# Optimization experiments

Hardware: AMD Instinct MI355X
Metric: run time of the kernel (lower is better)

The kernel has to match this reference:

```python
import jax, jax.numpy as jnp
import numpy as np

N_HEADS = 16
D_HEAD = 64
TAU = 30.0
NEG = -1e9


def setup_inputs() -> dict:
    key = jax.random.key(0)
    k1, k2, k3, k4 = jax.random.split(key, 4)
    B, L, D = 2, 2048, 1024
    scale = 1.0 / np.sqrt(D)
    return {
        "input": jax.random.normal(k1, (B, L, D), dtype=jnp.float32),
        "attention_mask": jnp.ones((B, L), dtype=jnp.int32),
        "W_Q": jax.random.normal(k2, (N_HEADS * D_HEAD, D), dtype=jnp.float32) * scale,
        "W_K": jax.random.normal(k3, (N_HEADS * D_HEAD, D), dtype=jnp.float32) * scale,
        "W_V": jax.random.normal(k4, (N_HEADS * D_HEAD, D), dtype=jnp.float32) * scale,
    }


def reference(input, attention_mask, W_Q, W_K, W_V):
    B, L, D = input.shape
    # fused QKV projection (F.linear: x @ W.T), split into heads: [B, H, L, Dh]
    def proj(W):
        return jnp.einsum('bld,ed->ble', input, W).reshape(B, L, N_HEADS, D_HEAD).transpose(0, 2, 1, 3)
    q, k, v = proj(W_Q), proj(W_K), proj(W_V)
    S = jnp.einsum('bhqd,bhkd->bhqk', q, k) / np.sqrt(D_HEAD)  # [B,H,L,L]
    S = TAU * jnp.tanh(S)
    causal = jnp.tril(jnp.ones((L, L), dtype=bool))            # True = keep
    keep = causal[None, None, :, :] & (attention_mask[:, None, None, :] != 0)
    S = jnp.where(keep, S, NEG)
    attn = jax.nn.softmax(S, axis=-1)
    out = jnp.einsum('bhqk,bhkd->bhqd', attn, v)
    return out.transpose(0, 2, 1, 3).reshape(B, L, N_HEADS * D_HEAD)
```

## Files before the change

kernel.cpp:

```cpp
#include <hip/hip_runtime.h>


typedef unsigned short u16;
typedef __bf16 bf16x8 __attribute__((ext_vector_type(8)));
typedef float f32x4 __attribute__((ext_vector_type(4)));

#define MFMA(a, b, c) __builtin_amdgcn_mfma_f32_16x16x32_bf16(a, b, c, 0, 0, 0)

__device__ __forceinline__ u16 bf16rne(float f) {
    unsigned int u = __float_as_uint(f);
    u += 0x7fffu + ((u >> 16) & 1u);
    return (u16)(u >> 16);
}
__device__ __forceinline__ float bf16f(u16 h) {
    return __uint_as_float(((unsigned int)h) << 16);
}
__device__ __forceinline__ void split1(float f, u16& hi, u16& lo) {
    hi = bf16rne(f);
    lo = bf16rne(f - bf16f(hi));
}

__device__ __forceinline__ void gl16(const u16* g, u16* l) {
    __builtin_amdgcn_global_load_lds(
        (const __attribute__((address_space(1))) unsigned int*)g,
        (__attribute__((address_space(3))) unsigned int*)l, 16, 0, 0);
}

__global__ __launch_bounds__(256) void presplit(
    const float* __restrict__ X, const float* __restrict__ Wq,
    const float* __restrict__ Wk, const float* __restrict__ Wv,
    u16* __restrict__ Xh, u16* __restrict__ Xl,
    u16* __restrict__ Wqh, u16* __restrict__ Wql,
    u16* __restrict__ Wkh, u16* __restrict__ Wkl,
    u16* __restrict__ Wvh)
{
    int i = blockIdx.x * 256 + threadIdx.x;
    const float* src; u16 *dh, *dl; int off;
    if (i < 1048576)      { src = X;  dh = Xh;  dl = Xl;      off = i; }
    else if (i < 1310720) { src = Wq; dh = Wqh; dl = Wql;     off = i - 1048576; }
    else if (i < 1572864) { src = Wk; dh = Wkh; dl = Wkl;     off = i - 1310720; }
    else                  { src = Wv; dh = Wvh; dl = nullptr; off = i - 1572864; }
    float4 v = ((const float4*)src)[off];
    ushort4 h, l;
    split1(v.x, h.x, l.x); split1(v.y, h.y, l.y);
    split1(v.z, h.z, l.z); split1(v.w, h.w, l.w);
    ((ushort4*)dh)[off] = h;
    if (dl) ((ushort4*)dl)[off] = l;
}

__global__ __launch_bounds__(256, 4) void qkv_gemm(
    const u16* __restrict__ Xh, const u16* __restrict__ Xl,
    const u16* __restrict__ Wqh, const u16* __restrict__ Wql,
    const u16* __restrict__ Wkh, const u16* __restrict__ Wkl,
    const u16* __restrict__ Wvh,
    u16* __restrict__ Qh, u16* __restrict__ Ql,
    u16* __restrict__ Kh, u16* __restrict__ Kl,
    u16* __restrict__ VT)
{
    __shared__ __align__(16) u16 Xhs[4096];
    __shared__ __align__(16) u16 Xls[4096];
    __shared__ __align__(16) u16 Whs[4096];
    __shared__ __align__(16) u16 Wls[4096];
    const int tid = threadIdx.x;
    const int wave = tid >> 6, lane = tid & 63, quad = lane >> 4, c16 = lane & 15;
    const int id = blockIdx.x;
    const int nb = (((id >> 3) % 3) << 3) | (id & 7);
    const int m0 = ((id >> 3) / 3) * 128;
    const int mat = nb >> 3;
    const int n0 = (nb & 7) * 128;
    const u16* Bh = (mat == 0) ? Wqh : ((mat == 1) ? Wkh : Wvh);
    const u16* Bl = (mat == 0) ? Wql : Wkl;
    const int nseg = (mat < 2) ? 3 : 1;
    const int wm = (wave >> 1) * 64, wn = (wave & 1) * 64;

    const int srow0 = wave * 32 + (lane >> 2), scol = (lane & 3) * 8;

    f32x4 acc[4][4];
#pragma unroll
    for (int i = 0; i < 4; i++)
#pragma unroll
        for (int j = 0; j < 4; j++) acc[i][j] = (f32x4){0.f, 0.f, 0.f, 0.f};

    for (int kt = 0; kt < 32; kt++) {
        const int kcol = kt * 32;
#pragma unroll
        for (int s = 0; s < 2; s++) {
            int row = srow0 + s * 16;
            size_t go = (size_t)row * 1024 + kcol + scol;
            int lo = row * 32 + scol;
            gl16(Xh + (size_t)m0 * 1024 + go, &Xhs[lo]);
            gl16(Bh + (size_t)n0 * 1024 + go, &Whs[lo]);
            if (nseg == 3) {
                gl16(Xl + (size_t)m0 * 1024 + go, &Xls[lo]);
                gl16(Bl + (size_t)n0 * 1024 + go, &Wls[lo]);
            }
        }
        __syncthreads();
        for (int seg = 0; seg < nseg; seg++) {
            const u16* ap = (seg < 2) ? Xhs : Xls;
            const u16* bp = (seg == 1) ? Wls : Whs;
            bf16x8 af[4], bfr[4];
#pragma unroll
            for (int mt = 0; mt < 4; mt++)
                af[mt] = *(const bf16x8*)&ap[(wm + mt * 16 + c16) * 32 + quad * 8];
#pragma unroll
            for (int nt = 0; nt < 4; nt++)
                bfr[nt] = *(const bf16x8*)&bp[(wn + nt * 16 + c16) * 32 + quad * 8];
#pragma unroll
            for (int mt = 0; mt < 4; mt++)
#pragma unroll
                for (int nt = 0; nt < 4; nt++)
                    acc[mt][nt] = MFMA(af[mt], bfr[nt], acc[mt][nt]);
        }
        __syncthreads();
    }

    const float scale = (mat == 0) ? 0.125f : 1.f;
#pragma unroll
    for (int mt = 0; mt < 4; mt++) {
#pragma unroll
        for (int nt = 0; nt < 4; nt++) {
#pragma unroll
            for (int reg = 0; reg < 4; reg++) {
                int mm = m0 + wm + mt * 16 + quad * 4 + reg;
                int n = n0 + wn + nt * 16 + c16;
                int b_ = mm >> 11, l = mm & 2047;
                int h = n >> 6, dh = n & 63;
                float v = acc[mt][nt][reg] * scale;
                if (mat == 2) {
                    VT[((b_ * 16 + h) * 64 + dh) * 2048 + l] = bf16rne(v);
                } else {
                    u16 hi, lo; split1(v, hi, lo);
                    int idx = ((b_ * 16 + h) * 2048 + l) * 64 + dh;
                    if (mat == 0) { Qh[idx] = hi; Ql[idx] = lo; }
                    else          { Kh[idx] = hi; Kl[idx] = lo; }
                }
            }
        }
    }
}

__global__ __launch_bounds__(256, 4) void attn(
    const u16* __restrict__ Qh, const u16* __restrict__ Ql,
    const u16* __restrict__ Kh, const u16* __restrict__ Kl,
    const u16* __restrict__ VT, const int* __restrict__ AM,
    u16* __restrict__ Op, float* __restrict__ Lp)
{
    __shared__ __align__(16) u16 Khs[2][4096];
    __shared__ __align__(16) u16 Kls[2][4096];
    __shared__ __align__(16) u16 Ps[4096];

    const int tid = threadIdx.x, wave = tid >> 6, lane = tid & 63;
    const int quad = lane >> 4, c16 = lane & 15;
    const int bh = blockIdx.x;
    const int pr = blockIdx.y;
    const int sp = blockIdx.z;
    const int b_ = bh >> 4;
    const size_t base = (size_t)bh * 2048 * 64;

    const int swsub[2] = { (wave * 2) >> 2, (wave * 2 + 1) >> 2 };
    const int swrow[2] = { ((wave * 2) & 3) * 16 + (lane >> 2), ((wave * 2 + 1) & 3) * 16 + (lane >> 2) };
    const int scol = (lane & 3) * 8;

    auto stageK = [&](int k0, int buf) {
        const u16* Kht = Kh + base + (size_t)k0 * 64;
        const u16* Klt = Kl + base + (size_t)k0 * 64;
#pragma unroll
        for (int s = 0; s < 2; s++) {
            int sub = swsub[s], row = swrow[s];
            int lo = sub * 2048 + row * 32 + scol;
            gl16(Kht + (size_t)row * 64 + sub * 32 + scol, &Khs[buf][lo]);
            gl16(Klt + (size_t)row * 64 + sub * 32 + scol, &Kls[buf][lo]);
        }
    };

    for (int tix = 0; tix < 2; ++tix) {
        const int qt = tix ? pr : 31 - pr;
        const int q0 = qt * 64;

        const size_t qrow = base + (size_t)(q0 + wave * 16 + c16) * 64 + quad * 8;
        bf16x8 qh0 = *(const bf16x8*)&Qh[qrow];
        bf16x8 qh1 = *(const bf16x8*)&Qh[qrow + 32];
        bf16x8 ql0 = *(const bf16x8*)&Ql[qrow];
        bf16x8 ql1 = *(const bf16x8*)&Ql[qrow + 32];

        float rsl[4] = {0.f, 0.f, 0.f, 0.f};
        f32x4 o[4];
#pragma unroll
        for (int r = 0; r < 4; r++) o[r] = (f32x4){0.f, 0.f, 0.f, 0.f};

        if (sp <= qt) {
            stageK(sp * 64, 0);
            int cur = 0;
            for (int kb = sp; kb <= qt; kb += 2) {
                const int k0 = kb * 64;
                __syncthreads();
                if (kb + 2 <= qt) stageK(k0 + 128, cur ^ 1);
                const int mkv = AM[b_ * 2048 + k0 + lane];
                const bool interior = (kb < qt);

                float p[4][4];
#pragma unroll
                for (int nt = 0; nt < 4; nt++) {
                    bf16x8 kh0 = *(const bf16x8*)&Khs[cur][(nt * 16 + c16) * 32 + quad * 8];
                    bf16x8 kh1 = *(const bf16x8*)&Khs[cur][2048 + (nt * 16 + c16) * 32 + quad * 8];
                    bf16x8 kl0 = *(const bf16x8*)&Kls[cur][(nt * 16 + c16) * 32 + quad * 8];
                    bf16x8 kl1 = *(const bf16x8*)&Kls[cur][2048 + (nt * 16 + c16) * 32 + quad * 8];
                    f32x4 sa = (f32x4){0.f, 0.f, 0.f, 0.f};
                    sa = MFMA(qh0, kh0, sa);
                    sa = MFMA(qh1, kh1, sa);
                    sa = MFMA(ql0, kh0, sa);
                    sa = MFMA(ql1, kh1, sa);
                    sa = MFMA(qh0, kl0, sa);
                    sa = MFMA(qh1, kl1, sa);
                    const int key = k0 + nt * 16 + c16;
                    const bool mok = (__shfl(mkv, nt * 16 + c16) != 0);
#pragma unroll
                    for (int reg = 0; reg < 4; reg++) {
                        int qg = q0 + wave * 16 + quad * 4 + reg;
                        float x = sa[reg];
                        float e1 = __expf(2.f * x);
                        float r  = __builtin_amdgcn_rcpf(e1 + 1.f);
                        float pv = __expf(-60.f * r);
                        bool keep = mok && (interior || key <= qg);
                        pv = keep ? pv : 0.f;
                        p[nt][reg] = pv;
                        rsl[reg] += pv;
                    }
                }

#pragma unroll
                for (int nt = 0; nt < 4; nt++) {
                    int kl_ = nt * 16 + c16, sub = kl_ >> 5, kc = kl_ & 31;
#pragma unroll
                    for (int reg = 0; reg < 4; reg++)
                        Ps[sub * 2048 + (wave * 16 + quad * 4 + reg) * 32 + kc] = bf16rne(p[nt][reg]);
                }
                bf16x8 p0 = *(const bf16x8*)&Ps[(wave * 16 + c16) * 32 + quad * 8];
                bf16x8 p1 = *(const bf16x8*)&Ps[2048 + (wave * 16 + c16) * 32 + quad * 8];

#pragma unroll
                for (int dt = 0; dt < 4; dt++) {
                    const size_t vrow = (size_t)(bh * 64 + dt * 16 + c16) * 2048 + k0 + quad * 8;
                    bf16x8 v0 = *(const bf16x8*)&VT[vrow];
                    bf16x8 v1 = *(const bf16x8*)&VT[vrow + 32];
                    o[dt] = MFMA(p0, v0, o[dt]);
                    o[dt] = MFMA(p1, v1, o[dt]);
                }
                cur ^= 1;
            }
        }
        __syncthreads();

        const size_t ob = ((size_t)(sp * 512 + bh * 16) + 0) * 0 +
                          ((size_t)((sp * 32 + 0) ) * 0);
        (void)ob;
        const size_t obase = (((size_t)sp * 1024 + (size_t)bh * 32 + qt) * 4096);
        const size_t lbase = (((size_t)sp * 1024 + (size_t)bh * 32 + qt) * 64);
        float lsum[4];
#pragma unroll
        for (int reg = 0; reg < 4; reg++) {
            float v = rsl[reg];
#pragma unroll
            for (int off = 1; off < 16; off <<= 1)
                v += __shfl_xor(v, off);
            lsum[reg] = v;
        }
        if (c16 == 0) {
#pragma unroll
            for (int reg = 0; reg < 4; reg++)
                Lp[lbase + wave * 16 + quad * 4 + reg] = lsum[reg];
        }
#pragma unroll
        for (int dt = 0; dt < 4; dt++)
#pragma unroll
            for (int reg = 0; reg < 4; reg++) {
                int row = wave * 16 + quad * 4 + reg;
                int d = dt * 16 + c16;
                Op[obase + row * 64 + d] = bf16rne(o[dt][reg]);
            }
    }
}

__global__ __launch_bounds__(256) void combine(
    const u16* __restrict__ Op, const float* __restrict__ Lp,
    float* __restrict__ Out)
{
    const int i = blockIdx.x * 256 + threadIdx.x;
    const size_t lin = (size_t)i * 4;
    const int d  = (int)(lin & 1023);
    const int h  = d >> 6, dd = d & 63;
    const int l  = (int)((lin >> 10) & 2047);
    const int b  = (int)(lin >> 21);
    const int qt = l >> 6, row = l & 63;
    const int bh = b * 16 + h;
    const size_t o0 = (((size_t)bh * 32 + qt) * 4096) + row * 64 + dd;
    const size_t o1 = o0 + (size_t)1024 * 4096;
    const size_t l0 = (((size_t)bh * 32 + qt) * 64) + row;
    ushort4 pa = *(const ushort4*)&Op[o0];
    ushort4 pb = *(const ushort4*)&Op[o1];
    float inv = __builtin_amdgcn_rcpf(Lp[l0] + Lp[l0 + 65536]);
    float4 r;
    r.x = (bf16f(pa.x) + bf16f(pb.x)) * inv;
    r.y = (bf16f(pa.y) + bf16f(pb.y)) * inv;
    r.z = (bf16f(pa.z) + bf16f(pb.z)) * inv;
    r.w = (bf16f(pa.w) + bf16f(pb.w)) * inv;
    *(float4*)&Out[lin] = r;
}

extern "C" void kernel_launch(void* const* d_in, const int* in_sizes, int n_in,
                              void* d_out, int out_size, void* d_ws, size_t ws_size,
                              hipStream_t stream) {
    const float* X  = (const float*)d_in[0];
    const int*   AM = (const int*)d_in[1];
    const float* Wq = (const float*)d_in[2];
    const float* Wk = (const float*)d_in[3];
    const float* Wv = (const float*)d_in[4];
    float* out = (float*)d_out;

    const size_t NE = (size_t)2 * 16 * 2048 * 64;
    const size_t WN = (size_t)1024 * 1024;
    u16* Qh  = (u16*)d_ws;
    u16* Ql  = Qh + NE;
    u16* Kh  = Ql + NE;
    u16* Kl  = Kh + NE;
    u16* VT  = Kl + NE;
    u16* Xh  = VT + NE;
    u16* Xl  = Xh + NE;
    u16* Wqh = Xl + NE;
    u16* Wql = Wqh + WN;
    u16* Wkh = Wql + WN;
    u16* Wkl = Wkh + WN;
    u16* Wvh = Wkl + WN;
    u16*   Op = Xh;
    float* Lp = (float*)Wqh;

    presplit<<<7168, 256, 0, stream>>>(X, Wq, Wk, Wv, Xh, Xl, Wqh, Wql, Wkh, Wkl, Wvh);
    qkv_gemm<<<768, 256, 0, stream>>>(Xh, Xl, Wqh, Wql, Wkh, Wkl, Wvh,
                                      Qh, Ql, Kh, Kl, VT);
    attn<<<dim3(32, 16, 2), 256, 0, stream>>>(Qh, Ql, Kh, Kl, VT, AM, Op, Lp);
    combine<<<4096, 256, 0, stream>>>(Op, Lp, out);
}
```

Baseline: 249.3 us.

## Stage V-transpose epilogue through LDS and prefetch V tiles before QK math

The QKV GEMM epilogue for V previously wrote scattered 2-byte stores into the transposed VT layout. It now packs bf16 pairs into LDS per wave and writes contiguous 16-byte rows. In the attention kernel, the V fragment global loads are issued at the top of each key-block iteration, before the QK MFMAs and softmax, so their latency overlaps with compute. The mask is also loaded per lane directly instead of through a shuffle. The cost is more live registers for the prefetched V fragments, which may reduce occupancy.

New measurement: 237.2 us. 4.9% less time.

```diff
diff --git a/kernel.cpp b/kernel.cpp
--- a/kernel.cpp
+++ b/kernel.cpp
@@ -1,4 +1,5 @@
 #include <hip/hip_runtime.h>
+#include <hip/hip_bf16.h>
 
 
 typedef unsigned short u16;
@@ -18,6 +19,10 @@
 __device__ __forceinline__ void split1(float f, u16& hi, u16& lo) {
     hi = bf16rne(f);
     lo = bf16rne(f - bf16f(hi));
+}
+__device__ __forceinline__ unsigned int pk2(float a, float b) {
+    __hip_bfloat162 t = __float22bfloat162_rn(float2{a, b});
+    return *(unsigned int*)&t;
 }
 
 __device__ __forceinline__ void gl16(const u16* g, u16* l) {
@@ -57,10 +62,11 @@
     u16* __restrict__ Kh, u16* __restrict__ Kl,
     u16* __restrict__ VT)
 {
-    __shared__ __align__(16) u16 Xhs[4096];
-    __shared__ __align__(16) u16 Xls[4096];
-    __shared__ __align__(16) u16 Whs[4096];
-    __shared__ __align__(16) u16 Wls[4096];
+    __shared__ __align__(16) u16 S[16384];
+    u16* const Xhs = &S[0];
+    u16* const Xls = &S[4096];
+    u16* const Whs = &S[8192];
+    u16* const Wls = &S[12288];
     const int tid = threadIdx.x;
     const int wave = tid >> 6, lane = tid & 63, quad = lane >> 4, c16 = lane & 15;
     const int id = blockIdx.x;
@@ -115,21 +121,44 @@
         __syncthreads();
     }
 
-    const float scale = (mat == 0) ? 0.125f : 1.f;
-#pragma unroll
-    for (int mt = 0; mt < 4; mt++) {
-#pragma unroll
-        for (int nt = 0; nt < 4; nt++) {
-#pragma unroll
-            for (int reg = 0; reg < 4; reg++) {
-                int mm = m0 + wm + mt * 16 + quad * 4 + reg;
-                int n = n0 + wn + nt * 16 + c16;
-                int b_ = mm >> 11, l = mm & 2047;
-                int h = n >> 6, dh = n & 63;
-                float v = acc[mt][nt][reg] * scale;
-                if (mat == 2) {
-                    VT[((b_ * 16 + h) * 64 + dh) * 2048 + l] = bf16rne(v);
-                } else {
+    if (mat == 2) {
+        u16* const T2 = &S[wave * 4096];
+        const int nglob = n0 + wn + lane;
+        const int hh = nglob >> 6, dh = nglob & 63;
+        const int bh64 = ((m0 >> 11) * 16 + hh) * 64 + dh;
+        u16* const vrow = VT + (size_t)bh64 * 2048 + (m0 & 2047) + wm;
+#pragma unroll
+        for (int half = 0; half < 2; half++) {
+#pragma unroll
+            for (int mt2 = 0; mt2 < 2; mt2++) {
+                int mt = half * 2 + mt2;
+#pragma unroll
+                for (int nt = 0; nt < 4; nt++) {
+                    uint2 d;
+                    d.x = pk2(acc[mt][nt][0], acc[mt][nt][1]);
+                    d.y = pk2(acc[mt][nt][2], acc[mt][nt][3]);
+                    *(uint2*)&T2[(nt * 16 + c16) * 40 + mt2 * 16 + quad * 4] = d;
+                }
+            }
+#pragma unroll
+            for (int c = 0; c < 4; c++) {
+                uint4 d = *(const uint4*)&T2[lane * 40 + c * 8];
+                *(uint4*)&vrow[half * 32 + c * 8] = d;
+            }
+        }
+    } else {
+        const float scale = (mat == 0) ? 0.125f : 1.f;
+#pragma unroll
+        for (int mt = 0; mt < 4; mt++) {
+#pragma unroll
+            for (int nt = 0; nt < 4; nt++) {
+#pragma unroll
+                for (int reg = 0; reg < 4; reg++) {
+                    int mm = m0 + wm + mt * 16 + quad * 4 + reg;
+                    int n = n0 + wn + nt * 16 + c16;
+                    int b_ = mm >> 11, l = mm & 2047;
+                    int h = n >> 6, dh = n & 63;
+                    float v = acc[mt][nt][reg] * scale;
                     u16 hi, lo; split1(v, hi, lo);
                     int idx = ((b_ * 16 + h) * 2048 + l) * 64 + dh;
                     if (mat == 0) { Qh[idx] = hi; Ql[idx] = lo; }
@@ -196,7 +225,18 @@
                 const int k0 = kb * 64;
                 __syncthreads();
                 if (kb + 2 <= qt) stageK(k0 + 128, cur ^ 1);
-                const int mkv = AM[b_ * 2048 + k0 + lane];
+
+                int mk[4];
+#pragma unroll
+                for (int nt = 0; nt < 4; nt++)
+                    mk[nt] = AM[b_ * 2048 + k0 + nt * 16 + c16];
+                bf16x8 vf[4][2];
+#pragma unroll
+                for (int dt = 0; dt < 4; dt++) {
+                    const size_t vrow = (size_t)(bh * 64 + dt * 16 + c16) * 2048 + k0 + quad * 8;
+                    vf[dt][0] = *(const bf16x8*)&VT[vrow];
+                    vf[dt][1] = *(const bf16x8*)&VT[vrow + 32];
+                }
                 const bool interior = (kb < qt);
 
                 float p[4][4];
@@ -214,7 +254,7 @@
                     sa = MFMA(qh0, kl0, sa);
                     sa = MFMA(qh1, kl1, sa);
                     const int key = k0 + nt * 16 + c16;
-                    const bool mok = (__shfl(mkv, nt * 16 + c16) != 0);
+                    const bool mok = (mk[nt] != 0);
 #pragma unroll
                     for (int reg = 0; reg < 4; reg++) {
                         int qg = q0 + wave * 16 + quad * 4 + reg;
@@ -238,23 +278,16 @@
                 }
                 bf16x8 p0 = *(const bf16x8*)&Ps[(wave * 16 + c16) * 32 + quad * 8];
                 bf16x8 p1 = *(const bf16x8*)&Ps[2048 + (wave * 16 + c16) * 32 + quad * 8];
-
 #pragma unroll
                 for (int dt = 0; dt < 4; dt++) {
-                    const size_t vrow = (size_t)(bh * 64 + dt * 16 + c16) * 2048 + k0 + quad * 8;
-                    bf16x8 v0 = *(const bf16x8*)&VT[vrow];
-                    bf16x8 v1 = *(const bf16x8*)&VT[vrow + 32];
-                    o[dt] = MFMA(p0, v0, o[dt]);
-                    o[dt] = MFMA(p1, v1, o[dt]);
+                    o[dt] = MFMA(p0, vf[dt][0], o[dt]);
+                    o[dt] = MFMA(p1, vf[dt][1], o[dt]);
                 }
                 cur ^= 1;
             }
         }
         __syncthreads();
 
-        const size_t ob = ((size_t)(sp * 512 + bh * 16) + 0) * 0 +
-                          ((size_t)((sp * 32 + 0) ) * 0);
-        (void)ob;
         const size_t obase = (((size_t)sp * 1024 + (size_t)bh * 32 + qt) * 4096);
         const size_t lbase = (((size_t)sp * 1024 + (size_t)bh * 32 + qt) * 64);
         float lsum[4];
```
